# Kernel tuning notes

Measured on AMD Instinct MI355X. Metric: run time of the kernel, lower is better.

The kernel has to match this reference:

```python
import jax, jax.numpy as jnp
import numpy as np

D_MODEL = 1024
NHEAD = 16
D_K = D_MODEL // NHEAD


def setup_inputs() -> dict:
    key = jax.random.key(0)
    ks = jax.random.split(key, 11)
    B, S = 4, 2048
    s = 1.0 / np.sqrt(D_MODEL)
    return {
        "query": jax.random.normal(ks[0], (B, S, D_MODEL), jnp.float32),
        "key": jax.random.normal(ks[1], (B, S, D_MODEL), jnp.float32),
        "value": jax.random.normal(ks[2], (B, S, D_MODEL), jnp.float32),
        "Wq": jax.random.normal(ks[3], (D_MODEL, D_MODEL), jnp.float32) * s,
        "bq": jnp.zeros((D_MODEL,), jnp.float32),
        "Wk": jax.random.normal(ks[4], (D_MODEL, D_MODEL), jnp.float32) * s,
        "bk": jnp.zeros((D_MODEL,), jnp.float32),
        "Wv": jax.random.normal(ks[5], (D_MODEL, D_MODEL), jnp.float32) * s,
        "bv": jnp.zeros((D_MODEL,), jnp.float32),
        "Wo": jax.random.normal(ks[6], (D_MODEL, D_MODEL), jnp.float32) * s,
        "bo": jnp.zeros((D_MODEL,), jnp.float32),
    }


def _split_heads(x):
    # [B, S, D] -> [B, H, S, d_k]
    B, S, _ = x.shape
    return x.reshape(B, S, NHEAD, D_K).transpose(0, 2, 1, 3)


def reference(query, key, value, Wq, bq, Wk, bk, Wv, bv, Wo, bo):
    # torch Linear: x @ W.T + b
    q = _split_heads(query @ Wq.T + bq)
    k = _split_heads(key @ Wk.T + bk)
    v = _split_heads(value @ Wv.T + bv)
    scale = 1.0 / np.sqrt(D_K).astype(np.float32)
    scores = jnp.einsum("bhqd,bhkd->bhqk", q, k) * scale
    attn = jax.nn.softmax(scores, axis=-1)  # dropout p=0 -> identity
    out = jnp.einsum("bhqk,bhkd->bhqd", attn, v)
    B, H, S, dk = out.shape
    out = out.transpose(0, 2, 1, 3).reshape(B, S, H * dk)
    return out @ Wo.T + bo
```

## Files before the change

### kernel.cpp

```cpp
#include <hip/hip_runtime.h>
#include <stdint.h>

#define DEVI static __device__ __forceinline__

typedef __attribute__((ext_vector_type(4))) float f32x4;
typedef __attribute__((ext_vector_type(16))) float f32x16;
typedef __attribute__((ext_vector_type(8))) __bf16 bf16x8;
typedef __attribute__((ext_vector_type(4))) uint16_t u16x4;
typedef uint16_t u16;

DEVI u16 f2bf(float f) {
  union { float f; uint32_t u; } v; v.f = f;
  uint32_t r = v.u + 0x7FFFu + ((v.u >> 16) & 1u);
  return (u16)(r >> 16);
}

DEVI f32x4 mfma16(bf16x8 a, bf16x8 b, f32x4 c) {
  return __builtin_amdgcn_mfma_f32_16x16x32_bf16(a, b, c, 0, 0, 0);
}

DEVI f32x16 mfma32(bf16x8 a, bf16x8 b, f32x16 c) {
  return __builtin_amdgcn_mfma_f32_32x32x16_bf16(a, b, c, 0, 0, 0);
}

DEVI void load_lds16(const void* g, void* l) {
  __builtin_amdgcn_global_load_lds(
      (const __attribute__((address_space(1))) void*)g,
      (__attribute__((address_space(3))) void*)l, 16, 0, 0);
}

DEVI bf16x8 lds_frag(const u16* p) { return *(const bf16x8*)p; }

DEVI f32x16 zero16() {
  f32x16 z;
#pragma unroll
  for (int i = 0; i < 16; ++i) z[i] = 0.f;
  return z;
}

DEVI float exp2_hw(float x) {
  float r;
  asm("v_exp_f32 %0, %1" : "=v"(r) : "v"(x));
  return r;
}

DEVI uint32_t cvtpk(float lo, float hi) {
  uint32_t r;
  asm("v_cvt_pk_bf16_f32 %0, %1, %2" : "=v"(r) : "v"(lo), "v"(hi));
  return r;
}

DEVI float max3f(float a, float b, float c) {
  float r;
  asm("v_max3_f32 %0, %1, %2, %3" : "=v"(r) : "v"(a), "v"(b), "v"(c));
  return r;
}

DEVI float partner_f(float x) { return __shfl_xor(x, 32, 64); }

DEVI void pswap_asm(uint32_t& a, uint32_t& b) {
  asm("v_permlane32_swap_b32 %0, %1" : "+v"(a), "+v"(b));
}

#define NBIG (4 * 2048 * 1024)
#define NW (1024 * 1024)

__global__ __launch_bounds__(256) void cvt_kernel(
    const float* q, const float* k, const float* v, const float* Wq,
    const float* Wk, const float* Wv, const float* Wo, u16* qb, u16* kb,
    u16* vb, u16* Wqb, u16* Wkb, u16* Wvb, u16* Wob) {
  const float* src;
  u16* dst;
  int n;
  switch (blockIdx.y) {
    case 0: src = q;  dst = qb;  n = NBIG; break;
    case 1: src = k;  dst = kb;  n = NBIG; break;
    case 2: src = v;  dst = vb;  n = NBIG; break;
    case 3: src = Wq; dst = Wqb; n = NW;   break;
    case 4: src = Wk; dst = Wkb; n = NW;   break;
    case 5: src = Wv; dst = Wvb; n = NW;   break;
    default: src = Wo; dst = Wob; n = NW;  break;
  }
  int i = (blockIdx.x * 256 + threadIdx.x) * 4;
  if (i >= n) return;
  float4 f = *(const float4*)&src[i];
  u16x4 o;
  o.x = f2bf(f.x); o.y = f2bf(f.y); o.z = f2bf(f.z); o.w = f2bf(f.w);
  *(u16x4*)&dst[i] = o;
}

DEVI void gemm_core_1024(const u16* __restrict__ A, const u16* __restrict__ Bm,
                         int bm, int bn, u16* As, u16* Bs, f32x4 acc[4][4]) {
  const int tid = threadIdx.x;
  const int w = tid >> 6, l = tid & 63;
  const int lr = l & 15, lg = l >> 4;
  const int wr = (w >> 1) * 64, wc = (w & 1) * 64;

  for (int i = 0; i < 4; ++i)
    for (int j = 0; j < 4; ++j) acc[i][j] = (f32x4){0.f, 0.f, 0.f, 0.f};

  const int c0 = 2 * w, c1 = 2 * w + 1;
  const u16* gA0 = A + (size_t)(bm * 128 + c0 * 16 + (l >> 2)) * 1024 + (l & 3) * 8;
  const u16* gA1 = A + (size_t)(bm * 128 + c1 * 16 + (l >> 2)) * 1024 + (l & 3) * 8;
  const u16* gB0 = Bm + (size_t)(bn * 128 + c0 * 16 + (l >> 2)) * 1024 + (l & 3) * 8;
  const u16* gB1 = Bm + (size_t)(bn * 128 + c1 * 16 + (l >> 2)) * 1024 + (l & 3) * 8;
  u16* lA0 = As + c0 * 512;
  u16* lA1 = As + c1 * 512;
  u16* lB0 = Bs + c0 * 512;
  u16* lB1 = Bs + c1 * 512;

  int aoff[4], boff[4];
#pragma unroll
  for (int mi = 0; mi < 4; ++mi) aoff[mi] = (wr + mi * 16 + lr) * 32 + lg * 8;
#pragma unroll
  for (int nj = 0; nj < 4; ++nj) boff[nj] = (wc + nj * 16 + lr) * 32 + lg * 8;

  for (int k0 = 0; k0 < 1024; k0 += 32) {
    load_lds16(gA0 + k0, lA0);
    load_lds16(gA1 + k0, lA1);
    load_lds16(gB0 + k0, lB0);
    load_lds16(gB1 + k0, lB1);
    __syncthreads();
    bf16x8 af[4], bff[4];
#pragma unroll
    for (int mi = 0; mi < 4; ++mi) af[mi] = lds_frag(&As[aoff[mi]]);
#pragma unroll
    for (int nj = 0; nj < 4; ++nj) bff[nj] = lds_frag(&Bs[boff[nj]]);
#pragma unroll
    for (int mi = 0; mi < 4; ++mi)
#pragma unroll
      for (int nj = 0; nj < 4; ++nj)
        acc[mi][nj] = mfma16(af[mi], bff[nj], acc[mi][nj]);
    __syncthreads();
  }
}

__global__ __launch_bounds__(256) void proj_kernel(
    const u16* qb, const u16* kb, const u16* vb, const u16* Wq, const u16* Wk,
    const u16* Wv, const float* bq, const float* bk, const float* bv, u16* Qp,
    u16* Kp, u16* Vt) {
  __shared__ __align__(16) u16 As[128 * 32];
  __shared__ __align__(16) u16 Bs[128 * 32];
  const int z = blockIdx.z;
  const u16* A = z == 0 ? qb : z == 1 ? kb : vb;
  const u16* W = z == 0 ? Wq : z == 1 ? Wk : Wv;
  const float* bias = z == 0 ? bq : z == 1 ? bk : bv;

  f32x4 acc[4][4];
  gemm_core_1024(A, W, blockIdx.x, blockIdx.y, As, Bs, acc);

  const int tid = threadIdx.x;
  const int w = tid >> 6, l = tid & 63;
  const int lr = l & 15, lg = l >> 4;
  const int wr = (w >> 1) * 64, wc = (w & 1) * 64;
  const int b = (blockIdx.x * 128) >> 11;

#pragma unroll
  for (int nj = 0; nj < 4; ++nj) {
    const int col = blockIdx.y * 128 + wc + nj * 16 + lr;
    const float bb = bias[col];
    const int h = col >> 6, d = col & 63;
#pragma unroll
    for (int mi = 0; mi < 4; ++mi) {
      const int m0 = blockIdx.x * 128 + wr + mi * 16 + lg * 4;
      const int s0 = m0 & 2047;
      if (z < 2) {
        u16* dst = (z == 0) ? Qp : Kp;
#pragma unroll
        for (int r = 0; r < 4; ++r)
          dst[(((size_t)(b * 16 + h) * 2048) + s0 + r) * 64 + d] =
              f2bf(acc[mi][nj][r] + bb);
      } else {
        u16x4 pk;
        pk.x = f2bf(acc[mi][nj][0] + bb);
        pk.y = f2bf(acc[mi][nj][1] + bb);
        pk.z = f2bf(acc[mi][nj][2] + bb);
        pk.w = f2bf(acc[mi][nj][3] + bb);
        *(u16x4*)&Vt[(((size_t)(b * 16 + h) * 64) + d) * 2048 + s0] = pk;
      }
    }
  }
}

__global__ __launch_bounds__(256) void outproj_kernel(const u16* O,
                                                      const u16* Wo,
                                                      const float* bo,
                                                      float* out) {
  __shared__ __align__(16) u16 As[128 * 32];
  __shared__ __align__(16) u16 Bs[128 * 32];
  f32x4 acc[4][4];
  gemm_core_1024(O, Wo, blockIdx.x, blockIdx.y, As, Bs, acc);

  const int tid = threadIdx.x;
  const int w = tid >> 6, l = tid & 63;
  const int lr = l & 15, lg = l >> 4;
  const int wr = (w >> 1) * 64, wc = (w & 1) * 64;
#pragma unroll
  for (int nj = 0; nj < 4; ++nj) {
    const int col = blockIdx.y * 128 + wc + nj * 16 + lr;
    const float bb = bo[col];
#pragma unroll
    for (int mi = 0; mi < 4; ++mi) {
      const int m0 = blockIdx.x * 128 + wr + mi * 16 + lg * 4;
#pragma unroll
      for (int r = 0; r < 4; ++r)
        out[(size_t)(m0 + r) * 1024 + col] = acc[mi][nj][r] + bb;
    }
  }
}

#define LDPK 72
#define NT 32
__global__ __launch_bounds__(512) void attn_kernel(const u16* Qp, const u16* Kp,
                                                   const u16* Vt, u16* Ob) {
  __shared__ __align__(16) u16 Kl[2][64 * LDPK];
  __shared__ __align__(16) u16 Vl[2][64 * LDPK];

  const int tid = threadIdx.x, w = tid >> 6, l = tid & 63;
  const int q = l & 31, hi = l >> 5;
  const int bh = blockIdx.y;
  const int q0 = blockIdx.x * 256 + w * 32;
  const u16* Qh = Qp + (size_t)bh * 2048 * 64;
  const u16* Kh = Kp + (size_t)bh * 2048 * 64;
  const u16* Vh = Vt + (size_t)bh * 64 * 2048;

  const float SC2 = 0.1803368801f;

  bf16x8 qf[4];
#pragma unroll
  for (int ds = 0; ds < 4; ++ds)
    qf[ds] = *(const bf16x8*)&Qh[(size_t)(q0 + q) * 64 + ds * 16 + hi * 8];

  f32x16 o0 = zero16(), o1 = zero16();
  float m = -1.0e30f, ln = 0.f;

  const int srow = tid >> 3, g0 = tid & 7;

  int koff[2][4], voff[2][4];
#pragma unroll
  for (int kb = 0; kb < 2; ++kb)
#pragma unroll
    for (int ds = 0; ds < 4; ++ds)
      koff[kb][ds] = (kb * 32 + q) * LDPK + ds * 16 + hi * 8;
#pragma unroll
  for (int db = 0; db < 2; ++db)
#pragma unroll
    for (int ks = 0; ks < 4; ++ks)
      voff[db][ks] = (db * 32 + q) * LDPK + ks * 16 + hi * 8;

  bf16x8 kv = *(const bf16x8*)&Kh[srow * 64 + g0 * 8];
  bf16x8 vv = *(const bf16x8*)&Vh[(size_t)srow * 2048 + g0 * 8];
  *(bf16x8*)&Kl[0][srow * LDPK + g0 * 8] = kv;
  *(bf16x8*)&Vl[0][srow * LDPK + g0 * 8] = vv;
  kv = *(const bf16x8*)&Kh[4096 + srow * 64 + g0 * 8];
  vv = *(const bf16x8*)&Vh[(size_t)srow * 2048 + 64 + g0 * 8];
  const u16* gk = Kh + 2 * 4096 + srow * 64 + g0 * 8;
  const u16* gv = Vh + (size_t)srow * 2048 + 2 * 64 + g0 * 8;
  __syncthreads();

  for (int kt = 0; kt < NT; ++kt) {
    const int cur = kt & 1;
    const u16* Kc = Kl[cur];
    const u16* Vc = Vl[cur];

    f32x16 c0 = zero16(), c1 = zero16();
    __builtin_amdgcn_s_setprio(1);
#pragma unroll
    for (int ds = 0; ds < 4; ++ds)
      c0 = mfma32(lds_frag(&Kc[koff[0][ds]]), qf[ds], c0);
#pragma unroll
    for (int ds = 0; ds < 4; ++ds)
      c1 = mfma32(lds_frag(&Kc[koff[1][ds]]), qf[ds], c1);
    __builtin_amdgcn_s_setprio(0);

    float tm[16];
#pragma unroll
    for (int r = 0; r < 16; ++r) tm[r] = fmaxf(c0[r], c1[r]);
    {
      const float m0_ = max3f(tm[0], tm[1], tm[2]);
      const float m1_ = max3f(tm[3], tm[4], tm[5]);
      const float m2_ = max3f(tm[6], tm[7], tm[8]);
      const float m3_ = max3f(tm[9], tm[10], tm[11]);
      const float m4_ = max3f(tm[12], tm[13], tm[14]);
      const float a_ = max3f(m0_, m1_, m2_);
      const float b_ = max3f(m3_, m4_, tm[15]);
      tm[0] = fmaxf(a_, b_);
    }
    const float mx = fmaxf(tm[0], partner_f(tm[0]));
    if (!__all(mx - m <= 64.0f)) {
      const float mnew = fmaxf(m, mx);
      const float a = exp2_hw((m - mnew) * SC2);
      m = mnew;
#pragma unroll
      for (int r = 0; r < 16; ++r) { o0[r] *= a; o1[r] *= a; }
      ln *= a;
    }
    const float m2 = m * SC2;
    float p0[16], p1[16];
#pragma unroll
    for (int r = 0; r < 16; ++r) {
      p0[r] = exp2_hw(__builtin_fmaf(c0[r], SC2, -m2));
      p1[r] = exp2_hw(__builtin_fmaf(c1[r], SC2, -m2));
    }
    float ts[16];
#pragma unroll
    for (int r = 0; r < 16; ++r) ts[r] = p0[r] + p1[r];
#pragma unroll
    for (int s = 8; s > 0; s >>= 1)
#pragma unroll
      for (int r = 0; r < s; ++r) ts[r] += ts[r + s];
    ln += ts[0] + partner_f(ts[0]);

    if (kt + 1 < NT) {
      *(bf16x8*)&Kl[cur ^ 1][srow * LDPK + g0 * 8] = kv;
      *(bf16x8*)&Vl[cur ^ 1][srow * LDPK + g0 * 8] = vv;
    }
    if (kt + 2 < NT) {
      kv = *(const bf16x8*)gk;
      vv = *(const bf16x8*)gv;
      gk += 4096; gv += 64;
    }

    uint32_t wv[16];
#pragma unroll
    for (int i = 0; i < 8; ++i) {
      wv[i]     = cvtpk(p0[2 * i], p0[2 * i + 1]);
      wv[8 + i] = cvtpk(p1[2 * i], p1[2 * i + 1]);
    }
    bf16x8 pa[4];
#pragma unroll
    for (int ks = 0; ks < 4; ++ks) {
      const int base = (ks >> 1) * 8 + 4 * (ks & 1);
      uint32_t x0 = wv[base],     y0 = wv[base + 2];
      uint32_t x1 = wv[base + 1], y1 = wv[base + 3];
      pswap_asm(x0, y0);
      pswap_asm(x1, y1);
      union { uint32_t u[4]; bf16x8 v; } cvt;
      cvt.u[0] = x0; cvt.u[1] = x1; cvt.u[2] = y0; cvt.u[3] = y1;
      pa[ks] = cvt.v;
    }

    __builtin_amdgcn_s_setprio(1);
#pragma unroll
    for (int ks = 0; ks < 4; ++ks)
      o0 = mfma32(lds_frag(&Vc[voff[0][ks]]), pa[ks], o0);
#pragma unroll
    for (int ks = 0; ks < 4; ++ks)
      o1 = mfma32(lds_frag(&Vc[voff[1][ks]]), pa[ks], o1);
    __builtin_amdgcn_s_setprio(0);

    __syncthreads();
  }

  const int b2 = bh >> 4, h = bh & 15;
  const float inv = 1.0f / ln;
  u16* orow = Ob + ((size_t)(b2 * 2048 + q0 + q)) * 1024 + h * 64;
#pragma unroll
  for (int g = 0; g < 4; ++g) {
    u16x4 pk;
    pk.x = f2bf(o0[4 * g + 0] * inv);
    pk.y = f2bf(o0[4 * g + 1] * inv);
    pk.z = f2bf(o0[4 * g + 2] * inv);
    pk.w = f2bf(o0[4 * g + 3] * inv);
    *(u16x4*)&orow[8 * g + 4 * hi] = pk;
  }
#pragma unroll
  for (int g = 0; g < 4; ++g) {
    u16x4 pk;
    pk.x = f2bf(o1[4 * g + 0] * inv);
    pk.y = f2bf(o1[4 * g + 1] * inv);
    pk.z = f2bf(o1[4 * g + 2] * inv);
    pk.w = f2bf(o1[4 * g + 3] * inv);
    *(u16x4*)&orow[32 + 8 * g + 4 * hi] = pk;
  }
}

extern "C" void kernel_launch(void* const* d_in, const int* in_sizes, int n_in,
                              void* d_out, int out_size, void* d_ws,
                              size_t ws_size, hipStream_t stream) {
  const float* q  = (const float*)d_in[0];
  const float* k  = (const float*)d_in[1];
  const float* v  = (const float*)d_in[2];
  const float* Wq = (const float*)d_in[3];
  const float* bq = (const float*)d_in[4];
  const float* Wk = (const float*)d_in[5];
  const float* bk = (const float*)d_in[6];
  const float* Wv = (const float*)d_in[7];
  const float* bv = (const float*)d_in[8];
  const float* Wo = (const float*)d_in[9];
  const float* bo = (const float*)d_in[10];
  float* out = (float*)d_out;

  u16* ws = (u16*)d_ws;
  u16* qb  = ws;
  u16* kb  = qb + NBIG;
  u16* vb  = kb + NBIG;
  u16* Wqb = vb + NBIG;
  u16* Wkb = Wqb + NW;
  u16* Wvb = Wkb + NW;
  u16* Wob = Wvb + NW;
  u16* Qp  = Wob + NW;
  u16* Kp  = Qp + NBIG;
  u16* Vt  = Kp + NBIG;
  u16* O   = qb;

  cvt_kernel<<<dim3(8192, 7, 1), 256, 0, stream>>>(q, k, v, Wq, Wk, Wv, Wo, qb,
                                                   kb, vb, Wqb, Wkb, Wvb, Wob);
  proj_kernel<<<dim3(64, 8, 3), 256, 0, stream>>>(qb, kb, vb, Wqb, Wkb, Wvb,
                                                  bq, bk, bv, Qp, Kp, Vt);
  attn_kernel<<<dim3(8, 64, 1), 512, 0, stream>>>(Qp, Kp, Vt, O);
  outproj_kernel<<<dim3(64, 8, 1), 256, 0, stream>>>(O, Wob, bo, out);
}
```

Baseline: 230.3 us.

## Double-buffer LDS tiles in projection GEMMs to overlap loads with MFMA

The shared GEMM core used by the QKV projection and output projection kernels now keeps two LDS buffers and prefetches the next K-slice while computing on the current one. This drops one barrier per iteration and is meant to hide global-to-LDS load latency behind the MFMA work. LDS use per block doubles to 32 KB, which may reduce occupancy. The overlap also depends on whether load_lds16 issues asynchronously or the compiler inserts waits before the compute.

```diff
diff --git a/kernel.cpp b/kernel.cpp
--- a/kernel.cpp
+++ b/kernel.cpp
@@ -89,8 +89,9 @@
   *(u16x4*)&dst[i] = o;
 }
 
-DEVI void gemm_core_1024(const u16* __restrict__ A, const u16* __restrict__ Bm,
-                         int bm, int bn, u16* As, u16* Bs, f32x4 acc[4][4]) {
+DEVI void gemm_core_1024_db(const u16* __restrict__ A,
+                            const u16* __restrict__ Bm, int bm, int bn,
+                            u16* As, u16* Bs, f32x4 acc[4][4]) {
   const int tid = threadIdx.x;
   const int w = tid >> 6, l = tid & 63;
   const int lr = l & 15, lg = l >> 4;
@@ -104,10 +105,7 @@
   const u16* gA1 = A + (size_t)(bm * 128 + c1 * 16 + (l >> 2)) * 1024 + (l & 3) * 8;
   const u16* gB0 = Bm + (size_t)(bn * 128 + c0 * 16 + (l >> 2)) * 1024 + (l & 3) * 8;
   const u16* gB1 = Bm + (size_t)(bn * 128 + c1 * 16 + (l >> 2)) * 1024 + (l & 3) * 8;
-  u16* lA0 = As + c0 * 512;
-  u16* lA1 = As + c1 * 512;
-  u16* lB0 = Bs + c0 * 512;
-  u16* lB1 = Bs + c1 * 512;
+  const int sA0 = c0 * 512, sA1 = c1 * 512;
 
   int aoff[4], boff[4];
 #pragma unroll
@@ -115,23 +113,35 @@
 #pragma unroll
   for (int nj = 0; nj < 4; ++nj) boff[nj] = (wc + nj * 16 + lr) * 32 + lg * 8;
 
+  load_lds16(gA0, As + sA0);
+  load_lds16(gA1, As + sA1);
+  load_lds16(gB0, Bs + sA0);
+  load_lds16(gB1, Bs + sA1);
+  __syncthreads();
+
+  int cur = 0;
   for (int k0 = 0; k0 < 1024; k0 += 32) {
-    load_lds16(gA0 + k0, lA0);
-    load_lds16(gA1 + k0, lA1);
-    load_lds16(gB0 + k0, lB0);
-    load_lds16(gB1 + k0, lB1);
-    __syncthreads();
+    const int nxt = cur ^ 1;
+    if (k0 + 32 < 1024) {
+      load_lds16(gA0 + k0 + 32, As + nxt * 4096 + sA0);
+      load_lds16(gA1 + k0 + 32, As + nxt * 4096 + sA1);
+      load_lds16(gB0 + k0 + 32, Bs + nxt * 4096 + sA0);
+      load_lds16(gB1 + k0 + 32, Bs + nxt * 4096 + sA1);
+    }
+    const u16* Ac = As + cur * 4096;
+    const u16* Bc = Bs + cur * 4096;
     bf16x8 af[4], bff[4];
 #pragma unroll
-    for (int mi = 0; mi < 4; ++mi) af[mi] = lds_frag(&As[aoff[mi]]);
-#pragma unroll
-    for (int nj = 0; nj < 4; ++nj) bff[nj] = lds_frag(&Bs[boff[nj]]);
+    for (int mi = 0; mi < 4; ++mi) af[mi] = lds_frag(&Ac[aoff[mi]]);
+#pragma unroll
+    for (int nj = 0; nj < 4; ++nj) bff[nj] = lds_frag(&Bc[boff[nj]]);
 #pragma unroll
     for (int mi = 0; mi < 4; ++mi)
 #pragma unroll
       for (int nj = 0; nj < 4; ++nj)
         acc[mi][nj] = mfma16(af[mi], bff[nj], acc[mi][nj]);
     __syncthreads();
+    cur = nxt;
   }
 }
 
@@ -139,15 +149,15 @@
     const u16* qb, const u16* kb, const u16* vb, const u16* Wq, const u16* Wk,
     const u16* Wv, const float* bq, const float* bk, const float* bv, u16* Qp,
     u16* Kp, u16* Vt) {
-  __shared__ __align__(16) u16 As[128 * 32];
-  __shared__ __align__(16) u16 Bs[128 * 32];
+  __shared__ __align__(16) u16 As[2 * 128 * 32];
+  __shared__ __align__(16) u16 Bs[2 * 128 * 32];
   const int z = blockIdx.z;
   const u16* A = z == 0 ? qb : z == 1 ? kb : vb;
   const u16* W = z == 0 ? Wq : z == 1 ? Wk : Wv;
   const float* bias = z == 0 ? bq : z == 1 ? bk : bv;
 
   f32x4 acc[4][4];
-  gemm_core_1024(A, W, blockIdx.x, blockIdx.y, As, Bs, acc);
+  gemm_core_1024_db(A, W, blockIdx.x, blockIdx.y, As, Bs, acc);
 
   const int tid = threadIdx.x;
   const int w = tid >> 6, l = tid & 63;
@@ -186,10 +196,10 @@
                                                       const u16* Wo,
                                                       const float* bo,
                                                       float* out) {
-  __shared__ __align__(16) u16 As[128 * 32];
-  __shared__ __align__(16) u16 Bs[128 * 32];
+  __shared__ __align__(16) u16 As[2 * 128 * 32];
+  __shared__ __align__(16) u16 Bs[2 * 128 * 32];
   f32x4 acc[4][4];
-  gemm_core_1024(O, Wo, blockIdx.x, blockIdx.y, As, Bs, acc);
+  gemm_core_1024_db(O, Wo, blockIdx.x, blockIdx.y, As, Bs, acc);
 
   const int tid = threadIdx.x;
   const int w = tid >> 6, l = tid & 63;
```

New measurement: 226.3 us. No clear change (-1.7%).
